# Performance work log

Measured on AMD Instinct MI355X. Metric: run time of the kernel, lower is better.

Reference implementation:

```python
import jax, jax.numpy as jnp
import numpy as np

WH, WW = 8, 8            # window size
N = WH * WW              # tokens per window = 64
DIM = 512
HEADS = 16
NW = 64                  # windows per image (mask batch)
B = 1024                 # total windows = 16 images * 64 windows
CPB_HIDDEN = 512


def _make_buffers():
    # relative coords table for CPB-MLP: [1, 2*WH-1, 2*WW-1, 2]
    rch = np.arange(-(WH - 1), WH, dtype=np.float32)
    rcw = np.arange(-(WW - 1), WW, dtype=np.float32)
    table = np.stack(np.meshgrid(rch, rcw, indexing='ij'), axis=-1)[None]
    table[..., 0] /= (WH - 1)
    table[..., 1] /= (WW - 1)
    table *= 8.0
    table = np.sign(table) * np.log2(np.abs(table) + 1.0) / 3.0
    # relative position index: [N, N]
    coords = np.stack(np.meshgrid(np.arange(WH), np.arange(WW), indexing='ij'), 0).reshape(2, -1)
    rel = coords[:, :, None] - coords[:, None, :]      # [2, N, N]
    rel = rel.transpose(1, 2, 0).astype(np.int64)
    rel[..., 0] += WH - 1
    rel[..., 1] += WW - 1
    rel[..., 0] *= 2 * WW - 1
    idx = rel.sum(-1)
    return jnp.asarray(table, jnp.float32), jnp.asarray(idx, jnp.int32)


def setup_inputs() -> dict:
    key = jax.random.key(0)
    ks = jax.random.split(key, 8)
    table, idx = _make_buffers()
    return {
        'x': jax.random.normal(ks[0], (B, N, DIM), jnp.float32),
        'mask': jax.random.normal(ks[1], (NW, N, N), jnp.float32),
        'qkv_w': jax.random.normal(ks[2], (3 * DIM, DIM), jnp.float32) * 0.02,
        'q_bias': jnp.zeros((DIM,), jnp.float32),
        'v_bias': jnp.zeros((DIM,), jnp.float32),
        'logit_scale': jnp.full((HEADS, 1, 1), np.log(10.0), jnp.float32),
        'cpb_w1': jax.random.normal(ks[3], (CPB_HIDDEN, 2), jnp.float32) * 0.02,
        'cpb_b1': jnp.zeros((CPB_HIDDEN,), jnp.float32),
        'cpb_w2': jax.random.normal(ks[4], (HEADS, CPB_HIDDEN), jnp.float32) * 0.02,
        'proj_w': jax.random.normal(ks[5], (DIM, DIM), jnp.float32) * 0.02,
        'proj_b': jnp.zeros((DIM,), jnp.float32),
        'rel_coords_table': table,
        'rel_pos_index': idx,
    }


def _l2norm(t):
    n = jnp.sqrt(jnp.sum(t * t, axis=-1, keepdims=True))
    return t / jnp.maximum(n, 1e-12)


def reference(x, mask, qkv_w, q_bias, v_bias, logit_scale, cpb_w1, cpb_b1,
              cpb_w2, proj_w, proj_b, rel_coords_table, rel_pos_index):
    Bq, Nq, C = x.shape
    qkv_b = jnp.concatenate([q_bias, jnp.zeros_like(v_bias), v_bias])
    qkv = x @ qkv_w.T + qkv_b                                  # [B, N, 3C]
    qkv = qkv.reshape(Bq, Nq, 3, HEADS, C // HEADS).transpose(2, 0, 3, 1, 4)
    q, k, v = qkv[0], qkv[1], qkv[2]                           # [B, H, N, D]
    attn = jnp.einsum('bhnd,bhmd->bhnm', _l2norm(q), _l2norm(k))
    scale = jnp.exp(jnp.minimum(logit_scale, jnp.log(jnp.float32(100.0))))
    attn = attn * scale                                        # [B, H, N, N]
    # CPB-MLP relative position bias
    hidden = jax.nn.relu(rel_coords_table @ cpb_w1.T + cpb_b1)  # [1, 2WH-1, 2WW-1, 512]
    bias_table = (hidden @ cpb_w2.T).reshape(-1, HEADS)         # [(2WH-1)(2WW-1), H]
    rel_bias = bias_table[rel_pos_index.reshape(-1)].reshape(Nq, Nq, HEADS)
    rel_bias = 16.0 * jax.nn.sigmoid(rel_bias.transpose(2, 0, 1))  # [H, N, N]
    attn = attn + rel_bias[None]
    nW = mask.shape[0]
    attn = attn.reshape(Bq // nW, nW, HEADS, Nq, Nq) + mask[None, :, None]
    attn = jax.nn.softmax(attn.reshape(Bq, HEADS, Nq, Nq), axis=-1)
    out = jnp.einsum('bhnm,bhmd->bhnd', attn, v)
    out = out.transpose(0, 2, 1, 3).reshape(Bq, Nq, C)
    return out @ proj_w.T + proj_b
```

## Files before the change

kernel.cpp:

```cpp
#include <hip/hip_runtime.h>
#include <hip/hip_bf16.h>

typedef __bf16 bf16;
typedef __bf16 bf16x4 __attribute__((ext_vector_type(4)));
typedef __bf16 bf16x8 __attribute__((ext_vector_type(8)));
typedef float floatx4 __attribute__((ext_vector_type(4)));

#define MFMA16(a, b, c) __builtin_amdgcn_mfma_f32_16x16x32_bf16((a), (b), (c), 0, 0, 0)

static constexpr long OFF_QKV   = 0;
static constexpr long OFF_XB    = 201326592;
static constexpr long OFF_WQKV  = 268435456;
static constexpr long OFF_WPROJ = 270008320;
static constexpr long OFF_BT    = 270532608;
static constexpr long OFF_RB    = 270548992;

__device__ __forceinline__ void load_lds16(const bf16* g, bf16* l) {
  __builtin_amdgcn_global_load_lds((const __attribute__((address_space(1))) void*)(g),
                                   (__attribute__((address_space(3))) void*)(l), 16, 0, 0);
}

__global__ __launch_bounds__(256) void cvt_f32_bf16(const float* __restrict__ src,
                                                    bf16* __restrict__ dst, int n8) {
  int i = blockIdx.x * 256 + threadIdx.x;
  if (i < n8) {
    const float4* s = (const float4*)src;
    float4 a = s[2 * i], b = s[2 * i + 1];
    bf16x8 o;
    o[0] = (bf16)a.x; o[1] = (bf16)a.y; o[2] = (bf16)a.z; o[3] = (bf16)a.w;
    o[4] = (bf16)b.x; o[5] = (bf16)b.y; o[6] = (bf16)b.z; o[7] = (bf16)b.w;
    ((bf16x8*)dst)[i] = o;
  }
}

__global__ __launch_bounds__(256) void cpb_mlp(const float* __restrict__ table,
                                               const float* __restrict__ w1,
                                               const float* __restrict__ b1,
                                               const float* __restrict__ w2,
                                               float* __restrict__ bias_table) {
  __shared__ float hid[512];
  const int e = blockIdx.x;
  const float t0 = table[e * 2 + 0], t1 = table[e * 2 + 1];
  for (int j = threadIdx.x; j < 512; j += 256) {
    float hv = t0 * w1[j * 2 + 0] + t1 * w1[j * 2 + 1] + b1[j];
    hid[j] = hv > 0.f ? hv : 0.f;
  }
  __syncthreads();
  const int hd = threadIdx.x >> 4, l = threadIdx.x & 15;
  float p = 0.f;
  for (int j = l; j < 512; j += 16) p += hid[j] * w2[hd * 512 + j];
  #pragma unroll
  for (int d = 8; d >= 1; d >>= 1) p += __shfl_xor(p, d, 16);
  if (l == 0) bias_table[e * 16 + hd] = p;
}

__global__ __launch_bounds__(256) void cpb_gather(const float* __restrict__ bias_table,
                                                  const int* __restrict__ idx,
                                                  float* __restrict__ rel_bias) {
  int f = blockIdx.x * 256 + threadIdx.x;
  int h = f >> 12, ij = f & 4095;
  float v = bias_table[idx[ij] * 16 + h];
  rel_bias[f] = 16.f / (1.f + __expf(-v));
}

template <int NN, bool QKV>
__global__ __launch_bounds__(256, 2) void gemm_bt(const bf16* __restrict__ A,
                                                  const bf16* __restrict__ Bt,
                                                  void* __restrict__ outv,
                                                  const float* __restrict__ bias_a,
                                                  const float* __restrict__ bias_b) {
  constexpr int K = 512;
  constexpr int KT = K / 64;
  constexpr int nblk = NN / 128;
  __shared__ alignas(16) bf16 As[2][128 * 64];
  __shared__ alignas(16) bf16 Bs[2][128 * 64];
  const int tid = threadIdx.x;
  const int lane = tid & 63;
  const int wv = tid >> 6;
  const int bid = blockIdx.x;
  const int xcd = bid & 7;
  const int g = bid >> 3;
  const int mb = xcd * 64 + g / nblk;
  const int nb = g % nblk;
  const long m0 = (long)mb * 128;
  const int n0 = nb * 128;
  const int wm = (wv & 1) * 64;
  const int wn = (wv >> 1) * 64;
  const int cl = lane & 15;
  const int cq = lane >> 4;

  const floatx4 fzero = {0.f, 0.f, 0.f, 0.f};
  floatx4 acc[4][4];
  #pragma unroll
  for (int i = 0; i < 4; ++i)
    #pragma unroll
    for (int j = 0; j < 4; ++j) acc[i][j] = fzero;

  int srow[4], sc8[4];
  #pragma unroll
  for (int r = 0; r < 4; ++r) {
    int s = r * 256 + tid;
    srow[r] = s >> 3;
    sc8[r] = (s & 7) ^ (srow[r] & 7);
  }
  const int wbase = tid & ~63;

  auto stage = [&](int buf, int kt) {
    const int k0 = kt * 64;
    #pragma unroll
    for (int r = 0; r < 4; ++r) {
      const bf16* ga = A + (m0 + srow[r]) * K + (k0 + sc8[r] * 8);
      load_lds16(ga, &As[buf][(r * 256 + wbase) * 8]);
      const bf16* gb = Bt + (long)(n0 + srow[r]) * K + (k0 + sc8[r] * 8);
      load_lds16(gb, &Bs[buf][(r * 256 + wbase) * 8]);
    }
  };

  stage(0, 0);
  __syncthreads();

  int cur = 0;
  for (int kt = 0; kt < KT; ++kt) {
    if (kt + 1 < KT) stage(cur ^ 1, kt + 1);
    #pragma unroll
    for (int kk = 0; kk < 2; ++kk) {
      bf16x8 af[4], bfr[4];
      const int gg = kk * 4 + cq;
      #pragma unroll
      for (int t = 0; t < 4; ++t) {
        const int mr = wm + t * 16 + cl;
        af[t] = *(const bf16x8*)&As[cur][(mr * 8 + (gg ^ (mr & 7))) * 8];
        const int nr = wn + t * 16 + cl;
        bfr[t] = *(const bf16x8*)&Bs[cur][(nr * 8 + (gg ^ (nr & 7))) * 8];
      }
      #pragma unroll
      for (int i = 0; i < 4; ++i)
        #pragma unroll
        for (int j = 0; j < 4; ++j)
          acc[i][j] = MFMA16(bfr[j], af[i], acc[i][j]);
    }
    __syncthreads();
    cur ^= 1;
  }

  const int cq4 = cq * 4;
  #pragma unroll
  for (int i = 0; i < 4; ++i) {
    const long m = m0 + wm + i * 16 + cl;
    #pragma unroll
    for (int j = 0; j < 4; ++j) {
      const int nbase = n0 + wn + j * 16 + cq4;
      if constexpr (QKV) {
        float4 bb = {0.f, 0.f, 0.f, 0.f};
        if (nbase < 512) bb = *(const float4*)&bias_a[nbase];
        else if (nbase >= 1024) bb = *(const float4*)&bias_b[nbase - 1024];
        bf16x4 o;
        o[0] = (bf16)(acc[i][j][0] + bb.x);
        o[1] = (bf16)(acc[i][j][1] + bb.y);
        o[2] = (bf16)(acc[i][j][2] + bb.z);
        o[3] = (bf16)(acc[i][j][3] + bb.w);
        *(bf16x4*)((bf16*)outv + m * NN + nbase) = o;
      } else {
        const float4 bb = *(const float4*)&bias_a[nbase];
        float4 o;
        o.x = acc[i][j][0] + bb.x;
        o.y = acc[i][j][1] + bb.y;
        o.z = acc[i][j][2] + bb.z;
        o.w = acc[i][j][3] + bb.w;
        *(float4*)((float*)outv + m * NN + nbase) = o;
      }
    }
  }
}

__global__ __launch_bounds__(256, 5) void attn_kernel(const bf16* __restrict__ qkv,
                                                      const float* __restrict__ mask,
                                                      const float* __restrict__ lscale,
                                                      const float* __restrict__ rel_bias,
                                                      bf16* __restrict__ out) {
  const int bid = blockIdx.x;
  const int xcd = bid & 7;
  const int t = bid >> 3;
  const int p = xcd + ((t >> 1) << 3);
  const int b = p >> 3;
  const int h = ((p & 7) << 1) | (t & 1);
  const int wi = b & 63;
  const int tid = threadIdx.x;
  const int lane = tid & 63;
  const int wv = tid >> 6;
  const int cl = lane & 15;
  const int cq = lane >> 4;

  __shared__ alignas(16) bf16 smem[12544];
  bf16* qh_s = smem;
  bf16* ql_s = smem + 2560;
  bf16* kh_s = smem + 5120;
  bf16* kl_s = smem + 7680;
  bf16* vT   = smem + 10240;
  bf16* ps   = smem;

  {
    const int r = tid >> 2, seg = tid & 3;
    const bf16* base = qkv + (long)(b * 64 + r) * 1536 + h * 32 + seg * 8;
    float f[8], ss;
    bf16x8 hi, lo;

    bf16x8 qv = *(const bf16x8*)(base);
    ss = 0.f;
    #pragma unroll
    for (int j = 0; j < 8; ++j) { f[j] = (float)qv[j]; ss += f[j] * f[j]; }
    ss += __shfl_xor(ss, 1, 4); ss += __shfl_xor(ss, 2, 4);
    float s1 = 1.f / fmaxf(sqrtf(ss), 1e-12f);
    #pragma unroll
    for (int j = 0; j < 8; ++j) {
      float xn = f[j] * s1;
      bf16 xh = (bf16)xn;
      hi[j] = xh; lo[j] = (bf16)(xn - (float)xh);
    }
    *(bf16x8*)&qh_s[r * 40 + seg * 8] = hi;
    *(bf16x8*)&ql_s[r * 40 + seg * 8] = lo;

    bf16x8 kv = *(const bf16x8*)(base + 512);
    ss = 0.f;
    #pragma unroll
    for (int j = 0; j < 8; ++j) { f[j] = (float)kv[j]; ss += f[j] * f[j]; }
    ss += __shfl_xor(ss, 1, 4); ss += __shfl_xor(ss, 2, 4);
    s1 = 1.f / fmaxf(sqrtf(ss), 1e-12f);
    #pragma unroll
    for (int j = 0; j < 8; ++j) {
      float xn = f[j] * s1;
      bf16 xh = (bf16)xn;
      hi[j] = xh; lo[j] = (bf16)(xn - (float)xh);
    }
    *(bf16x8*)&kh_s[r * 40 + seg * 8] = hi;
    *(bf16x8*)&kl_s[r * 40 + seg * 8] = lo;

    bf16x8 vv = *(const bf16x8*)(base + 1024);
    #pragma unroll
    for (int j = 0; j < 8; ++j) vT[(seg * 8 + j) * 72 + r] = vv[j];
  }
  __syncthreads();

  const float sc = __expf(fminf(lscale[h], 4.6051701859880914f));

  const int mrow = wv * 16 + cl;
  const bf16x8 aqh = *(const bf16x8*)&qh_s[mrow * 40 + cq * 8];
  const bf16x8 aql = *(const bf16x8*)&ql_s[mrow * 40 + cq * 8];
  floatx4 sacc[4];
  #pragma unroll
  for (int nt = 0; nt < 4; ++nt) {
    const int nr = nt * 16 + cl;
    const bf16x8 bkh = *(const bf16x8*)&kh_s[nr * 40 + cq * 8];
    const bf16x8 bkl = *(const bf16x8*)&kl_s[nr * 40 + cq * 8];
    floatx4 a = {0.f, 0.f, 0.f, 0.f};
    a = MFMA16(aql, bkh, a);
    a = MFMA16(aqh, bkl, a);
    a = MFMA16(aqh, bkh, a);
    sacc[nt] = a;
  }
  __syncthreads();

  float pw[4][4];
  #pragma unroll
  for (int rg = 0; rg < 4; ++rg) {
    const int row = wv * 16 + cq * 4 + rg;
    const float* rbp = rel_bias + h * 4096 + row * 64;
    const float* mkp = mask + wi * 4096 + row * 64;
    float mxv = -1e30f;
    #pragma unroll
    for (int nt = 0; nt < 4; ++nt) {
      float s = sacc[nt][rg] * sc + rbp[nt * 16 + cl] + mkp[nt * 16 + cl];
      pw[rg][nt] = s;
      mxv = fmaxf(mxv, s);
    }
    #pragma unroll
    for (int d = 8; d >= 1; d >>= 1) mxv = fmaxf(mxv, __shfl_xor(mxv, d, 16));
    float sm = 0.f;
    #pragma unroll
    for (int nt = 0; nt < 4; ++nt) {
      float e = __expf(pw[rg][nt] - mxv);
      pw[rg][nt] = e;
      sm += e;
    }
    #pragma unroll
    for (int d = 8; d >= 1; d >>= 1) sm += __shfl_xor(sm, d, 16);
    const float inv = 1.f / sm;
    #pragma unroll
    for (int nt = 0; nt < 4; ++nt)
      ps[row * 72 + nt * 16 + cl] = (bf16)(pw[rg][nt] * inv);
  }

  floatx4 oacc[2];
  oacc[0] = (floatx4){0.f, 0.f, 0.f, 0.f};
  oacc[1] = (floatx4){0.f, 0.f, 0.f, 0.f};
  #pragma unroll
  for (int ks = 0; ks < 2; ++ks) {
    const bf16x8 ap = *(const bf16x8*)&ps[(wv * 16 + cl) * 72 + ks * 32 + cq * 8];
    #pragma unroll
    for (int nt = 0; nt < 2; ++nt) {
      const bf16x8 bv = *(const bf16x8*)&vT[(nt * 16 + cl) * 72 + ks * 32 + cq * 8];
      oacc[nt] = MFMA16(bv, ap, oacc[nt]);
    }
  }
  const long obase = (long)(b * 64 + wv * 16 + cl) * 512 + h * 32 + cq * 4;
  #pragma unroll
  for (int nt = 0; nt < 2; ++nt) {
    bf16x4 o;
    #pragma unroll
    for (int r = 0; r < 4; ++r) o[r] = (bf16)oacc[nt][r];
    *(bf16x4*)&out[obase + nt * 16] = o;
  }
}

extern "C" void kernel_launch(void* const* d_in, const int* in_sizes, int n_in,
                              void* d_out, int out_size, void* d_ws, size_t ws_size,
                              hipStream_t stream) {
  const float* x      = (const float*)d_in[0];
  const float* mask   = (const float*)d_in[1];
  const float* qkv_w  = (const float*)d_in[2];
  const float* q_bias = (const float*)d_in[3];
  const float* v_bias = (const float*)d_in[4];
  const float* lsc    = (const float*)d_in[5];
  const float* cpb_w1 = (const float*)d_in[6];
  const float* cpb_b1 = (const float*)d_in[7];
  const float* cpb_w2 = (const float*)d_in[8];
  const float* proj_w = (const float*)d_in[9];
  const float* proj_b = (const float*)d_in[10];
  const float* table  = (const float*)d_in[11];
  const int*   relidx = (const int*)d_in[12];

  char* ws = (char*)d_ws;
  bf16* qkvb   = (bf16*)(ws + OFF_QKV);
  bf16* xb     = (bf16*)(ws + OFF_XB);
  bf16* wqkv   = (bf16*)(ws + OFF_WQKV);
  bf16* wproj  = (bf16*)(ws + OFF_WPROJ);
  float* btab  = (float*)(ws + OFF_BT);
  float* rbias = (float*)(ws + OFF_RB);

  cvt_f32_bf16<<<16384, 256, 0, stream>>>(x, xb, 65536 * 512 / 8);
  cvt_f32_bf16<<<384, 256, 0, stream>>>(qkv_w, wqkv, 1536 * 512 / 8);
  cvt_f32_bf16<<<128, 256, 0, stream>>>(proj_w, wproj, 512 * 512 / 8);
  cpb_mlp<<<225, 256, 0, stream>>>(table, cpb_w1, cpb_b1, cpb_w2, btab);
  cpb_gather<<<256, 256, 0, stream>>>(btab, relidx, rbias);

  gemm_bt<1536, true><<<6144, 256, 0, stream>>>(xb, wqkv, (void*)qkvb, q_bias, v_bias);
  attn_kernel<<<16384, 256, 0, stream>>>(qkvb, mask, lsc, rbias, xb);
  gemm_bt<512, false><<<2048, 256, 0, stream>>>(xb, wproj, d_out, proj_b, nullptr);
}
```

Baseline: 559.4 us.

## Enlarge GEMM tile to 256x128 with 512 threads and triple-buffered pipeline

The bf16 GEMM kernel moves from 128x128 tiles on 256 threads to 256x128 tiles on 512 threads (8 waves). It now uses a three-stage LDS ring with explicit vmcnt waits and raw s_barrier in place of a double buffer with __syncthreads. It also raises wave priority around the MFMA block. The aim is better reuse of B tiles and more load/compute overlap. The cost is 144KB of LDS per block, which likely permits only one block per CU despite the launch bound of 2, and the block-to-tile mapping changes with it.

```diff
diff --git a/kernel.cpp b/kernel.cpp
--- a/kernel.cpp
+++ b/kernel.cpp
@@ -64,7 +64,7 @@
 }
 
 template <int NN, bool QKV>
-__global__ __launch_bounds__(256, 2) void gemm_bt(const bf16* __restrict__ A,
+__global__ __launch_bounds__(512, 2) void gemm_bt(const bf16* __restrict__ A,
                                                   const bf16* __restrict__ Bt,
                                                   void* __restrict__ outv,
                                                   const float* __restrict__ bias_a,
@@ -72,20 +72,20 @@
   constexpr int K = 512;
   constexpr int KT = K / 64;
   constexpr int nblk = NN / 128;
-  __shared__ alignas(16) bf16 As[2][128 * 64];
-  __shared__ alignas(16) bf16 Bs[2][128 * 64];
+  __shared__ alignas(16) bf16 As[3][256 * 64];
+  __shared__ alignas(16) bf16 Bs[3][128 * 64];
   const int tid = threadIdx.x;
   const int lane = tid & 63;
   const int wv = tid >> 6;
   const int bid = blockIdx.x;
   const int xcd = bid & 7;
   const int g = bid >> 3;
-  const int mb = xcd * 64 + g / nblk;
-  const int nb = g % nblk;
-  const long m0 = (long)mb * 128;
+  const int mb = xcd * 32 + (g & 31);
+  const int nb = g >> 5;
+  const long m0 = (long)mb * 256;
   const int n0 = nb * 128;
-  const int wm = (wv & 1) * 64;
-  const int wn = (wv >> 1) * 64;
+  const int wm = (wv & 3) * 64;
+  const int wn = (wv >> 2) * 64;
   const int cl = lane & 15;
   const int cq = lane >> 4;
 
@@ -99,7 +99,7 @@
   int srow[4], sc8[4];
   #pragma unroll
   for (int r = 0; r < 4; ++r) {
-    int s = r * 256 + tid;
+    int s = r * 512 + tid;
     srow[r] = s >> 3;
     sc8[r] = (s & 7) ^ (srow[r] & 7);
   }
@@ -109,19 +109,17 @@
     const int k0 = kt * 64;
     #pragma unroll
     for (int r = 0; r < 4; ++r) {
-      const bf16* ga = A + (m0 + srow[r]) * K + (k0 + sc8[r] * 8);
-      load_lds16(ga, &As[buf][(r * 256 + wbase) * 8]);
+      const bf16* ga = A + (m0 + srow[r]) * (long)K + (k0 + sc8[r] * 8);
+      load_lds16(ga, &As[buf][(r * 512 + wbase) * 8]);
+    }
+    #pragma unroll
+    for (int r = 0; r < 2; ++r) {
       const bf16* gb = Bt + (long)(n0 + srow[r]) * K + (k0 + sc8[r] * 8);
-      load_lds16(gb, &Bs[buf][(r * 256 + wbase) * 8]);
+      load_lds16(gb, &Bs[buf][(r * 512 + wbase) * 8]);
     }
   };
 
-  stage(0, 0);
-  __syncthreads();
-
-  int cur = 0;
-  for (int kt = 0; kt < KT; ++kt) {
-    if (kt + 1 < KT) stage(cur ^ 1, kt + 1);
+  auto compute = [&](int buf) {
     #pragma unroll
     for (int kk = 0; kk < 2; ++kk) {
       bf16x8 af[4], bfr[4];
@@ -129,18 +127,36 @@
       #pragma unroll
       for (int t = 0; t < 4; ++t) {
         const int mr = wm + t * 16 + cl;
-        af[t] = *(const bf16x8*)&As[cur][(mr * 8 + (gg ^ (mr & 7))) * 8];
+        af[t] = *(const bf16x8*)&As[buf][(mr * 8 + (gg ^ (mr & 7))) * 8];
         const int nr = wn + t * 16 + cl;
-        bfr[t] = *(const bf16x8*)&Bs[cur][(nr * 8 + (gg ^ (nr & 7))) * 8];
+        bfr[t] = *(const bf16x8*)&Bs[buf][(nr * 8 + (gg ^ (nr & 7))) * 8];
       }
+      __builtin_amdgcn_s_setprio(1);
       #pragma unroll
       for (int i = 0; i < 4; ++i)
         #pragma unroll
         for (int j = 0; j < 4; ++j)
           acc[i][j] = MFMA16(bfr[j], af[i], acc[i][j]);
-    }
-    __syncthreads();
-    cur ^= 1;
+      __builtin_amdgcn_s_setprio(0);
+    }
+  };
+
+  stage(0, 0);
+  stage(1, 1);
+  asm volatile("s_waitcnt vmcnt(6)" ::: "memory");
+  __builtin_amdgcn_s_barrier();
+
+  #pragma unroll
+  for (int kt = 0; kt < KT; ++kt) {
+    if (kt + 2 < KT) stage((kt + 2) % 3, kt + 2);
+    __builtin_amdgcn_sched_barrier(0);
+    compute(kt % 3);
+    __builtin_amdgcn_sched_barrier(0);
+    if (kt + 2 < KT)
+      asm volatile("s_waitcnt vmcnt(6)" ::: "memory");
+    else if (kt + 1 < KT)
+      asm volatile("s_waitcnt vmcnt(0)" ::: "memory");
+    if (kt + 1 < KT) __builtin_amdgcn_s_barrier();
   }
 
   const int cq4 = cq * 4;
@@ -343,7 +359,7 @@
   cpb_mlp<<<225, 256, 0, stream>>>(table, cpb_w1, cpb_b1, cpb_w2, btab);
   cpb_gather<<<256, 256, 0, stream>>>(btab, relidx, rbias);
 
-  gemm_bt<1536, true><<<6144, 256, 0, stream>>>(xb, wqkv, (void*)qkvb, q_bias, v_bias);
+  gemm_bt<1536, true><<<256 * 12, 512, 0, stream>>>(xb, wqkv, (void*)qkvb, q_bias, v_bias);
   attn_kernel<<<16384, 256, 0, stream>>>(qkvb, mask, lsc, rbias, xb);
-  gemm_bt<512, false><<<2048, 256, 0, stream>>>(xb, wproj, d_out, proj_b, nullptr);
-}
+  gemm_bt<512, false><<<256 * 4, 512, 0, stream>>>(xb, wproj, d_out, proj_b, nullptr);
+}
```

Result: slower. 608.7 us (+8.8%).

## Halve GEMM K-tile to 32 for higher occupancy with explicit waits and setprio

Applied to the files above, without the earlier changes.

Shrinks the GEMM K-tile from 64 to 32, halving LDS per block (with a new 4-way XOR swizzle) and raising launch bounds to 4 waves per SIMD to allow more resident blocks. The main loop is fully unrolled, replaces __syncthreads with explicit vmcnt waits plus barriers, and raises wave priority around the MFMA cluster. The aim is better latency hiding through occupancy. The cost is twice as many barriers and shorter compute phases between loads, and the tighter register budget could spill the 64 accumulator registers.

```diff
diff --git a/kernel.cpp b/kernel.cpp
--- a/kernel.cpp
+++ b/kernel.cpp
@@ -64,16 +64,16 @@
 }
 
 template <int NN, bool QKV>
-__global__ __launch_bounds__(256, 2) void gemm_bt(const bf16* __restrict__ A,
+__global__ __launch_bounds__(256, 4) void gemm_bt(const bf16* __restrict__ A,
                                                   const bf16* __restrict__ Bt,
                                                   void* __restrict__ outv,
                                                   const float* __restrict__ bias_a,
                                                   const float* __restrict__ bias_b) {
   constexpr int K = 512;
-  constexpr int KT = K / 64;
+  constexpr int KT = K / 32;
   constexpr int nblk = NN / 128;
-  __shared__ alignas(16) bf16 As[2][128 * 64];
-  __shared__ alignas(16) bf16 Bs[2][128 * 64];
+  __shared__ alignas(16) bf16 As[2][128 * 32];
+  __shared__ alignas(16) bf16 Bs[2][128 * 32];
   const int tid = threadIdx.x;
   const int lane = tid & 63;
   const int wv = tid >> 6;
@@ -88,6 +88,7 @@
   const int wn = (wv >> 1) * 64;
   const int cl = lane & 15;
   const int cq = lane >> 4;
+  const int wbase = tid & ~63;
 
   const floatx4 fzero = {0.f, 0.f, 0.f, 0.f};
   floatx4 acc[4][4];
@@ -96,51 +97,53 @@
     #pragma unroll
     for (int j = 0; j < 4; ++j) acc[i][j] = fzero;
 
-  int srow[4], sc8[4];
-  #pragma unroll
-  for (int r = 0; r < 4; ++r) {
-    int s = r * 256 + tid;
-    srow[r] = s >> 3;
-    sc8[r] = (s & 7) ^ (srow[r] & 7);
-  }
-  const int wbase = tid & ~63;
-
-  auto stage = [&](int buf, int kt) {
-    const int k0 = kt * 64;
-    #pragma unroll
-    for (int r = 0; r < 4; ++r) {
-      const bf16* ga = A + (m0 + srow[r]) * K + (k0 + sc8[r] * 8);
+  int srow[2], sgl[2];
+  #pragma unroll
+  for (int r = 0; r < 2; ++r) {
+    const int s = r * 256 + tid;
+    srow[r] = s >> 2;
+    sgl[r] = (s & 3) ^ ((s >> 2) & 3);
+  }
+  const int sx = cq ^ (cl & 3);
+
+  auto stage = [&](int buf, int j) {
+    const int k0 = j * 32;
+    #pragma unroll
+    for (int r = 0; r < 2; ++r) {
+      const bf16* ga = A + (m0 + srow[r]) * (long)K + (k0 + sgl[r] * 8);
       load_lds16(ga, &As[buf][(r * 256 + wbase) * 8]);
-      const bf16* gb = Bt + (long)(n0 + srow[r]) * K + (k0 + sc8[r] * 8);
+      const bf16* gb = Bt + (long)(n0 + srow[r]) * K + (k0 + sgl[r] * 8);
       load_lds16(gb, &Bs[buf][(r * 256 + wbase) * 8]);
     }
   };
 
   stage(0, 0);
-  __syncthreads();
-
-  int cur = 0;
-  for (int kt = 0; kt < KT; ++kt) {
-    if (kt + 1 < KT) stage(cur ^ 1, kt + 1);
-    #pragma unroll
-    for (int kk = 0; kk < 2; ++kk) {
-      bf16x8 af[4], bfr[4];
-      const int gg = kk * 4 + cq;
+  asm volatile("s_waitcnt vmcnt(0)" ::: "memory");
+  __builtin_amdgcn_s_barrier();
+
+  #pragma unroll
+  for (int h = 0; h < KT; ++h) {
+    const int buf = h & 1;
+    if (h + 1 < KT) stage(buf ^ 1, h + 1);
+    bf16x8 af[4], bfr[4];
+    #pragma unroll
+    for (int t = 0; t < 4; ++t) {
+      const int mr = wm + t * 16 + cl;
+      af[t] = *(const bf16x8*)&As[buf][(mr * 4 + sx) * 8];
+      const int nr = wn + t * 16 + cl;
+      bfr[t] = *(const bf16x8*)&Bs[buf][(nr * 4 + sx) * 8];
+    }
+    __builtin_amdgcn_s_setprio(1);
+    #pragma unroll
+    for (int i = 0; i < 4; ++i)
       #pragma unroll
-      for (int t = 0; t < 4; ++t) {
-        const int mr = wm + t * 16 + cl;
-        af[t] = *(const bf16x8*)&As[cur][(mr * 8 + (gg ^ (mr & 7))) * 8];
-        const int nr = wn + t * 16 + cl;
-        bfr[t] = *(const bf16x8*)&Bs[cur][(nr * 8 + (gg ^ (nr & 7))) * 8];
-      }
-      #pragma unroll
-      for (int i = 0; i < 4; ++i)
-        #pragma unroll
-        for (int j = 0; j < 4; ++j)
-          acc[i][j] = MFMA16(bfr[j], af[i], acc[i][j]);
-    }
-    __syncthreads();
-    cur ^= 1;
+      for (int j = 0; j < 4; ++j)
+        acc[i][j] = MFMA16(bfr[j], af[i], acc[i][j]);
+    __builtin_amdgcn_s_setprio(0);
+    if (h + 1 < KT) {
+      asm volatile("s_waitcnt vmcnt(0)" ::: "memory");
+      __builtin_amdgcn_s_barrier();
+    }
   }
 
   const int cq4 = cq * 4;
```

Result: no change. 552.3 us (-1.3%).
